# Kernel tuning notes

Hardware: AMD Instinct MI355X
Metric: run time of the kernel (lower is better)

The kernel has to match this reference:

```python
import jax, jax.numpy as jnp
import numpy as np

B, H, S, D = 4, 16, 1024, 64

def setup_inputs() -> dict:
    key = jax.random.key(0)
    kq, kk, kv, kb, km = jax.random.split(key, 5)
    return {
        "q": jax.random.normal(kq, (B, H, S, D), dtype=jnp.float32),
        "k": jax.random.normal(kk, (B, H, S, D), dtype=jnp.float32),
        "v": jax.random.normal(kv, (B, H, S, D), dtype=jnp.float32),
        "add_attn": jax.random.normal(kb, (B, 1, S, S), dtype=jnp.float32),
        "mask": jax.random.randint(km, (B, 1, 1, S), 0, 2, dtype=jnp.int32),
    }

def reference(q, k, v, add_attn, mask):
    d_emb = q.shape[-1]
    scale = 1.0 / jnp.sqrt(jnp.float32(d_emb)).astype(q.dtype)
    # scores: [B,H,Sq,Sk]
    attn = jnp.einsum('bhqd,bhkd->bhqk', q * scale, k)
    attn = attn + add_attn
    attn = jnp.where(mask == 0, jnp.asarray(-1e9, attn.dtype), attn)
    attn = jax.nn.softmax(attn, axis=-1)  # dropout with p=0 is identity
    output = jnp.einsum('bhqk,bhkd->bhqd', attn, v)
    return (output, attn)
```

## Files before the change

kernel.cpp:

```cpp
#include <hip/hip_runtime.h>
#include <math.h>

#define BB 4
#define HH 16
#define SS 1024
#define DD 64
#define QT 16
#define NKW 4
#define KPW 256

typedef __attribute__((ext_vector_type(8))) short bf16x8;
typedef __attribute__((ext_vector_type(4))) float f32x4;

static __device__ inline unsigned short f2bf(float f) {
    unsigned int u = __float_as_uint(f);
    u += 0x7fff + ((u >> 16) & 1);
    return (unsigned short)(u >> 16);
}

__global__ __launch_bounds__(256) void convert_qk(const float* __restrict__ q,
                                                  const float* __restrict__ k,
                                                  unsigned short* __restrict__ qb,
                                                  unsigned short* __restrict__ kb) {
    const int idx = blockIdx.x * 256 + threadIdx.x;
    float4 qv = ((const float4*)q)[idx];
    float4 kv = ((const float4*)k)[idx];
    ushort4 qo = make_ushort4(f2bf(qv.x), f2bf(qv.y), f2bf(qv.z), f2bf(qv.w));
    ushort4 ko = make_ushort4(f2bf(kv.x), f2bf(kv.y), f2bf(kv.z), f2bf(kv.w));
    ((ushort4*)qb)[idx] = qo;
    ((ushort4*)kb)[idx] = ko;
}

__global__ __launch_bounds__(256) void transpose_v(const float* __restrict__ v,
                                                   unsigned short* __restrict__ vt) {
    const int idx = blockIdx.x * 256 + threadIdx.x;
    const int k  = (idx & 255) * 4;
    const int d  = (idx >> 8) & 63;
    const int bh = idx >> 14;
    const float* vb = v + (size_t)bh * SS * DD;
    ushort4 o = make_ushort4(f2bf(vb[(size_t)(k + 0) * DD + d]),
                             f2bf(vb[(size_t)(k + 1) * DD + d]),
                             f2bf(vb[(size_t)(k + 2) * DD + d]),
                             f2bf(vb[(size_t)(k + 3) * DD + d]));
    ((ushort4*)vt)[idx] = o;
}

__global__ __launch_bounds__(256) void attn_mfma(
    const unsigned short* __restrict__ qb,
    const unsigned short* __restrict__ kb,
    const unsigned short* __restrict__ vtb,
    const float* __restrict__ add_attn,
    const int*   __restrict__ mask,
    float* __restrict__ out,
    float* __restrict__ attn_out)
{
    const int qt = blockIdx.x, h = blockIdx.y, b = blockIdx.z;
    const int bh = b * HH + h;
    const int tid = threadIdx.x;
    const int wave = tid >> 6;
    const int lane = tid & 63;
    const int col  = lane & 15;
    const int quad = lane >> 4;

    __shared__ unsigned short p_tile[NKW][QT][KPW + 8];
    __shared__ float red_m[NKW][QT];
    __shared__ float red_l[NKW][QT];
    __shared__ float o_part[NKW][QT][DD];

    const int q0  = qt * QT;
    const int wk0 = wave * KPW;

    const unsigned short* qrow = qb + ((size_t)bh * SS + q0 + col) * DD + quad * 8;
    const bf16x8 aq0 = *(const bf16x8*)(qrow);
    const bf16x8 aq1 = *(const bf16x8*)(qrow + 32);

    const unsigned short* kbb = kb + (size_t)bh * SS * DD;
    const float* bias = add_attn + ((size_t)b * SS + q0) * SS;
    const int*   mrow = mask + b * SS;

    float s[16][4];
#pragma unroll
    for (int t = 0; t < 16; ++t) {
        const int k0 = wk0 + t * 16;
        const unsigned short* kr = kbb + (size_t)(k0 + col) * DD + quad * 8;
        bf16x8 bk0 = *(const bf16x8*)(kr);
        bf16x8 bk1 = *(const bf16x8*)(kr + 32);
        f32x4 acc = {0.f, 0.f, 0.f, 0.f};
        acc = __builtin_amdgcn_mfma_f32_16x16x32_bf16(aq0, bk0, acc, 0, 0, 0);
        acc = __builtin_amdgcn_mfma_f32_16x16x32_bf16(aq1, bk1, acc, 0, 0, 0);
        const int kidx = k0 + col;
        const int mv = mrow[kidx];
#pragma unroll
        for (int r = 0; r < 4; ++r) {
            const int qr = quad * 4 + r;
            float sv = acc[r] * 0.125f + bias[(size_t)qr * SS + kidx];
            s[t][r] = (mv == 0) ? -1e9f : sv;
        }
    }

    float mx[4];
#pragma unroll
    for (int r = 0; r < 4; ++r) {
        float m = s[0][r];
#pragma unroll
        for (int t = 1; t < 16; ++t) m = fmaxf(m, s[t][r]);
        m = fmaxf(m, __shfl_xor(m, 1));
        m = fmaxf(m, __shfl_xor(m, 2));
        m = fmaxf(m, __shfl_xor(m, 4));
        m = fmaxf(m, __shfl_xor(m, 8));
        mx[r] = m;
    }
    if (col == 0) {
#pragma unroll
        for (int r = 0; r < 4; ++r) red_m[wave][quad * 4 + r] = mx[r];
    }
    __syncthreads();
    float mf[4];
#pragma unroll
    for (int r = 0; r < 4; ++r) {
        const int qr = quad * 4 + r;
        mf[r] = fmaxf(fmaxf(red_m[0][qr], red_m[1][qr]),
                      fmaxf(red_m[2][qr], red_m[3][qr]));
    }

    float ls[4] = {0.f, 0.f, 0.f, 0.f};
#pragma unroll
    for (int t = 0; t < 16; ++t) {
#pragma unroll
        for (int r = 0; r < 4; ++r) {
            float e = __expf(s[t][r] - mf[r]);
            s[t][r] = e;
            ls[r] += e;
        }
    }
#pragma unroll
    for (int r = 0; r < 4; ++r) {
        float l = ls[r];
        l += __shfl_xor(l, 1);
        l += __shfl_xor(l, 2);
        l += __shfl_xor(l, 4);
        l += __shfl_xor(l, 8);
        ls[r] = l;
    }
    if (col == 0) {
#pragma unroll
        for (int r = 0; r < 4; ++r) red_l[wave][quad * 4 + r] = ls[r];
    }
    __syncthreads();
    float inv[4];
#pragma unroll
    for (int r = 0; r < 4; ++r) {
        const int qr = quad * 4 + r;
        inv[r] = 1.0f / (red_l[0][qr] + red_l[1][qr] + red_l[2][qr] + red_l[3][qr]);
    }

    float* arow = attn_out + ((size_t)bh * SS + q0) * SS;
#pragma unroll
    for (int t = 0; t < 16; ++t) {
#pragma unroll
        for (int r = 0; r < 4; ++r) {
            const int qr = quad * 4 + r;
            float p = s[t][r] * inv[r];
            arow[(size_t)qr * SS + wk0 + t * 16 + col] = p;
            p_tile[wave][qr][t * 16 + col] = f2bf(p);
        }
    }

    const unsigned short* vt = vtb + (size_t)bh * DD * SS;
    f32x4 oacc[4];
#pragma unroll
    for (int dc = 0; dc < 4; ++dc) oacc[dc] = (f32x4){0.f, 0.f, 0.f, 0.f};
#pragma unroll
    for (int c = 0; c < 8; ++c) {
        bf16x8 ap = *(const bf16x8*)(&p_tile[wave][col][c * 32 + quad * 8]);
#pragma unroll
        for (int dc = 0; dc < 4; ++dc) {
            const unsigned short* vr =
                vt + (size_t)(dc * 16 + col) * SS + wk0 + c * 32 + quad * 8;
            bf16x8 bv = *(const bf16x8*)(vr);
            oacc[dc] = __builtin_amdgcn_mfma_f32_16x16x32_bf16(ap, bv, oacc[dc], 0, 0, 0);
        }
    }
#pragma unroll
    for (int dc = 0; dc < 4; ++dc)
#pragma unroll
        for (int r = 0; r < 4; ++r)
            o_part[wave][quad * 4 + r][dc * 16 + col] = oacc[dc][r];
    __syncthreads();

    for (int i = tid; i < QT * DD; i += 256) {
        const int qr = i >> 6, d = i & 63;
        out[((size_t)bh * SS + q0 + qr) * DD + d] =
            o_part[0][qr][d] + o_part[1][qr][d] + o_part[2][qr][d] + o_part[3][qr][d];
    }
}

extern "C" void kernel_launch(void* const* d_in, const int* in_sizes, int n_in,
                              void* d_out, int out_size, void* d_ws, size_t ws_size,
                              hipStream_t stream) {
    const float* q        = (const float*)d_in[0];
    const float* k        = (const float*)d_in[1];
    const float* v        = (const float*)d_in[2];
    const float* add_attn = (const float*)d_in[3];
    const int*   mask     = (const int*)d_in[4];

    float* out      = (float*)d_out;
    float* attn_out = (float*)d_out + (size_t)BB * HH * SS * DD;

    const size_t nelem = (size_t)BB * HH * SS * DD;
    unsigned short* qb  = (unsigned short*)d_ws;
    unsigned short* kbb = qb + nelem;
    unsigned short* vtb = kbb + nelem;

    convert_qk<<<dim3(nelem / 4 / 256), dim3(256), 0, stream>>>(q, k, qb, kbb);
    transpose_v<<<dim3(nelem / 4 / 256), dim3(256), 0, stream>>>(v, vtb);

    dim3 grid(SS / QT, HH, BB);
    attn_mfma<<<grid, dim3(256), 0, stream>>>(qb, kbb, vtb, add_attn, mask, out, attn_out);
}
```

Baseline: 474.4 us.

## Reuse bias/mask across heads per block, tile V transpose via LDS, nontemporal stores

Each attention block now handles 8 heads of one batch. The add_attn bias and mask tile is loaded into registers once and reused across those heads instead of being re-read per head. The V transpose goes through a shared-memory tile, so global reads and writes are coalesced. Outputs use nontemporal stores, and launch bounds request 2 blocks per CU. The grid shrinks to 64x2x4 blocks, which reduces parallelism, and the extra br[16][4] registers raise register pressure.

```diff
diff --git a/kernel.cpp b/kernel.cpp
--- a/kernel.cpp
+++ b/kernel.cpp
@@ -8,6 +8,7 @@
 #define QT 16
 #define NKW 4
 #define KPW 256
+#define HPB 8
 
 typedef __attribute__((ext_vector_type(8))) short bf16x8;
 typedef __attribute__((ext_vector_type(4))) float f32x4;
@@ -33,19 +34,36 @@
 
 __global__ __launch_bounds__(256) void transpose_v(const float* __restrict__ v,
                                                    unsigned short* __restrict__ vt) {
-    const int idx = blockIdx.x * 256 + threadIdx.x;
-    const int k  = (idx & 255) * 4;
-    const int d  = (idx >> 8) & 63;
-    const int bh = idx >> 14;
-    const float* vb = v + (size_t)bh * SS * DD;
-    ushort4 o = make_ushort4(f2bf(vb[(size_t)(k + 0) * DD + d]),
-                             f2bf(vb[(size_t)(k + 1) * DD + d]),
-                             f2bf(vb[(size_t)(k + 2) * DD + d]),
-                             f2bf(vb[(size_t)(k + 3) * DD + d]));
-    ((ushort4*)vt)[idx] = o;
-}
-
-__global__ __launch_bounds__(256) void attn_mfma(
+    __shared__ unsigned short t[DD][258];
+    const int bh = blockIdx.y;
+    const int k0 = blockIdx.x * 256;
+    const float* vb = v + ((size_t)bh * SS + k0) * DD;
+#pragma unroll
+    for (int j = 0; j < 16; ++j) {
+        const int f   = j * 256 + threadIdx.x;
+        const int row = f >> 4;
+        const int d4  = (f & 15) << 2;
+        float4 x = ((const float4*)vb)[f];
+        t[d4 + 0][row] = f2bf(x.x);
+        t[d4 + 1][row] = f2bf(x.y);
+        t[d4 + 2][row] = f2bf(x.z);
+        t[d4 + 3][row] = f2bf(x.w);
+    }
+    __syncthreads();
+    unsigned short* vo = vt + (size_t)bh * DD * SS + k0;
+#pragma unroll
+    for (int j = 0; j < 8; ++j) {
+        const int f  = j * 256 + threadIdx.x;
+        const int d  = f >> 5;
+        const int k8 = (f & 31) << 3;
+        const unsigned int* lp = (const unsigned int*)&t[d][k8];
+        uint4 w;
+        w.x = lp[0]; w.y = lp[1]; w.z = lp[2]; w.w = lp[3];
+        *(uint4*)(vo + (size_t)d * SS + k8) = w;
+    }
+}
+
+__global__ __launch_bounds__(256, 2) void attn_mfma(
     const unsigned short* __restrict__ qb,
     const unsigned short* __restrict__ kb,
     const unsigned short* __restrict__ vtb,
@@ -54,8 +72,7 @@
     float* __restrict__ out,
     float* __restrict__ attn_out)
 {
-    const int qt = blockIdx.x, h = blockIdx.y, b = blockIdx.z;
-    const int bh = b * HH + h;
+    const int qt = blockIdx.x, hg = blockIdx.y, b = blockIdx.z;
     const int tid = threadIdx.x;
     const int wave = tid >> 6;
     const int lane = tid & 63;
@@ -70,128 +87,143 @@
     const int q0  = qt * QT;
     const int wk0 = wave * KPW;
 
-    const unsigned short* qrow = qb + ((size_t)bh * SS + q0 + col) * DD + quad * 8;
-    const bf16x8 aq0 = *(const bf16x8*)(qrow);
-    const bf16x8 aq1 = *(const bf16x8*)(qrow + 32);
-
-    const unsigned short* kbb = kb + (size_t)bh * SS * DD;
     const float* bias = add_attn + ((size_t)b * SS + q0) * SS;
     const int*   mrow = mask + b * SS;
-
-    float s[16][4];
+    float br[16][4];
 #pragma unroll
     for (int t = 0; t < 16; ++t) {
-        const int k0 = wk0 + t * 16;
-        const unsigned short* kr = kbb + (size_t)(k0 + col) * DD + quad * 8;
-        bf16x8 bk0 = *(const bf16x8*)(kr);
-        bf16x8 bk1 = *(const bf16x8*)(kr + 32);
-        f32x4 acc = {0.f, 0.f, 0.f, 0.f};
-        acc = __builtin_amdgcn_mfma_f32_16x16x32_bf16(aq0, bk0, acc, 0, 0, 0);
-        acc = __builtin_amdgcn_mfma_f32_16x16x32_bf16(aq1, bk1, acc, 0, 0, 0);
-        const int kidx = k0 + col;
+        const int kidx = wk0 + t * 16 + col;
         const int mv = mrow[kidx];
 #pragma unroll
         for (int r = 0; r < 4; ++r) {
             const int qr = quad * 4 + r;
-            float sv = acc[r] * 0.125f + bias[(size_t)qr * SS + kidx];
-            s[t][r] = (mv == 0) ? -1e9f : sv;
-        }
-    }
-
-    float mx[4];
-#pragma unroll
-    for (int r = 0; r < 4; ++r) {
-        float m = s[0][r];
-#pragma unroll
-        for (int t = 1; t < 16; ++t) m = fmaxf(m, s[t][r]);
-        m = fmaxf(m, __shfl_xor(m, 1));
-        m = fmaxf(m, __shfl_xor(m, 2));
-        m = fmaxf(m, __shfl_xor(m, 4));
-        m = fmaxf(m, __shfl_xor(m, 8));
-        mx[r] = m;
-    }
-    if (col == 0) {
-#pragma unroll
-        for (int r = 0; r < 4; ++r) red_m[wave][quad * 4 + r] = mx[r];
-    }
-    __syncthreads();
-    float mf[4];
-#pragma unroll
-    for (int r = 0; r < 4; ++r) {
-        const int qr = quad * 4 + r;
-        mf[r] = fmaxf(fmaxf(red_m[0][qr], red_m[1][qr]),
-                      fmaxf(red_m[2][qr], red_m[3][qr]));
-    }
-
-    float ls[4] = {0.f, 0.f, 0.f, 0.f};
-#pragma unroll
-    for (int t = 0; t < 16; ++t) {
-#pragma unroll
-        for (int r = 0; r < 4; ++r) {
-            float e = __expf(s[t][r] - mf[r]);
-            s[t][r] = e;
-            ls[r] += e;
-        }
-    }
-#pragma unroll
-    for (int r = 0; r < 4; ++r) {
-        float l = ls[r];
-        l += __shfl_xor(l, 1);
-        l += __shfl_xor(l, 2);
-        l += __shfl_xor(l, 4);
-        l += __shfl_xor(l, 8);
-        ls[r] = l;
-    }
-    if (col == 0) {
-#pragma unroll
-        for (int r = 0; r < 4; ++r) red_l[wave][quad * 4 + r] = ls[r];
-    }
-    __syncthreads();
-    float inv[4];
-#pragma unroll
-    for (int r = 0; r < 4; ++r) {
-        const int qr = quad * 4 + r;
-        inv[r] = 1.0f / (red_l[0][qr] + red_l[1][qr] + red_l[2][qr] + red_l[3][qr]);
-    }
-
-    float* arow = attn_out + ((size_t)bh * SS + q0) * SS;
-#pragma unroll
-    for (int t = 0; t < 16; ++t) {
+            float bv = bias[(size_t)qr * SS + kidx];
+            br[t][r] = mv ? bv : -1e9f;
+        }
+    }
+
+    for (int hi = 0; hi < HPB; ++hi) {
+        const int h  = hg * HPB + hi;
+        const int bh = b * HH + h;
+
+        const unsigned short* qrow = qb + ((size_t)bh * SS + q0 + col) * DD + quad * 8;
+        const bf16x8 aq0 = *(const bf16x8*)(qrow);
+        const bf16x8 aq1 = *(const bf16x8*)(qrow + 32);
+
+        const unsigned short* kbb = kb + (size_t)bh * SS * DD;
+
+        float s[16][4];
+#pragma unroll
+        for (int t = 0; t < 16; ++t) {
+            const int k0 = wk0 + t * 16;
+            const unsigned short* kr = kbb + (size_t)(k0 + col) * DD + quad * 8;
+            bf16x8 bk0 = *(const bf16x8*)(kr);
+            bf16x8 bk1 = *(const bf16x8*)(kr + 32);
+            f32x4 acc = {0.f, 0.f, 0.f, 0.f};
+            acc = __builtin_amdgcn_mfma_f32_16x16x32_bf16(aq0, bk0, acc, 0, 0, 0);
+            acc = __builtin_amdgcn_mfma_f32_16x16x32_bf16(aq1, bk1, acc, 0, 0, 0);
+#pragma unroll
+            for (int r = 0; r < 4; ++r)
+                s[t][r] = acc[r] * 0.125f + br[t][r];
+        }
+
+        float mx[4];
+#pragma unroll
+        for (int r = 0; r < 4; ++r) {
+            float m = s[0][r];
+#pragma unroll
+            for (int t = 1; t < 16; ++t) m = fmaxf(m, s[t][r]);
+            m = fmaxf(m, __shfl_xor(m, 1));
+            m = fmaxf(m, __shfl_xor(m, 2));
+            m = fmaxf(m, __shfl_xor(m, 4));
+            m = fmaxf(m, __shfl_xor(m, 8));
+            mx[r] = m;
+        }
+        if (col == 0) {
+#pragma unroll
+            for (int r = 0; r < 4; ++r) red_m[wave][quad * 4 + r] = mx[r];
+        }
+        __syncthreads();
+        float mf[4];
 #pragma unroll
         for (int r = 0; r < 4; ++r) {
             const int qr = quad * 4 + r;
-            float p = s[t][r] * inv[r];
-            arow[(size_t)qr * SS + wk0 + t * 16 + col] = p;
-            p_tile[wave][qr][t * 16 + col] = f2bf(p);
-        }
-    }
-
-    const unsigned short* vt = vtb + (size_t)bh * DD * SS;
-    f32x4 oacc[4];
-#pragma unroll
-    for (int dc = 0; dc < 4; ++dc) oacc[dc] = (f32x4){0.f, 0.f, 0.f, 0.f};
-#pragma unroll
-    for (int c = 0; c < 8; ++c) {
-        bf16x8 ap = *(const bf16x8*)(&p_tile[wave][col][c * 32 + quad * 8]);
-#pragma unroll
-        for (int dc = 0; dc < 4; ++dc) {
-            const unsigned short* vr =
-                vt + (size_t)(dc * 16 + col) * SS + wk0 + c * 32 + quad * 8;
-            bf16x8 bv = *(const bf16x8*)(vr);
-            oacc[dc] = __builtin_amdgcn_mfma_f32_16x16x32_bf16(ap, bv, oacc[dc], 0, 0, 0);
-        }
-    }
-#pragma unroll
-    for (int dc = 0; dc < 4; ++dc)
-#pragma unroll
-        for (int r = 0; r < 4; ++r)
-            o_part[wave][quad * 4 + r][dc * 16 + col] = oacc[dc][r];
-    __syncthreads();
-
-    for (int i = tid; i < QT * DD; i += 256) {
-        const int qr = i >> 6, d = i & 63;
-        out[((size_t)bh * SS + q0 + qr) * DD + d] =
-            o_part[0][qr][d] + o_part[1][qr][d] + o_part[2][qr][d] + o_part[3][qr][d];
+            mf[r] = fmaxf(fmaxf(red_m[0][qr], red_m[1][qr]),
+                          fmaxf(red_m[2][qr], red_m[3][qr]));
+        }
+
+        float ls[4] = {0.f, 0.f, 0.f, 0.f};
+#pragma unroll
+        for (int t = 0; t < 16; ++t) {
+#pragma unroll
+            for (int r = 0; r < 4; ++r) {
+                float e = __expf(s[t][r] - mf[r]);
+                s[t][r] = e;
+                ls[r] += e;
+            }
+        }
+#pragma unroll
+        for (int r = 0; r < 4; ++r) {
+            float l = ls[r];
+            l += __shfl_xor(l, 1);
+            l += __shfl_xor(l, 2);
+            l += __shfl_xor(l, 4);
+            l += __shfl_xor(l, 8);
+            ls[r] = l;
+        }
+        if (col == 0) {
+#pragma unroll
+            for (int r = 0; r < 4; ++r) red_l[wave][quad * 4 + r] = ls[r];
+        }
+        __syncthreads();
+        float inv[4];
+#pragma unroll
+        for (int r = 0; r < 4; ++r) {
+            const int qr = quad * 4 + r;
+            inv[r] = 1.0f / (red_l[0][qr] + red_l[1][qr] + red_l[2][qr] + red_l[3][qr]);
+        }
+
+        float* arow = attn_out + ((size_t)bh * SS + q0) * SS;
+#pragma unroll
+        for (int t = 0; t < 16; ++t) {
+#pragma unroll
+            for (int r = 0; r < 4; ++r) {
+                const int qr = quad * 4 + r;
+                float p = s[t][r] * inv[r];
+                __builtin_nontemporal_store(p, &arow[(size_t)qr * SS + wk0 + t * 16 + col]);
+                p_tile[wave][qr][t * 16 + col] = f2bf(p);
+            }
+        }
+
+        const unsigned short* vt = vtb + (size_t)bh * DD * SS;
+        f32x4 oacc[4];
+#pragma unroll
+        for (int dc = 0; dc < 4; ++dc) oacc[dc] = (f32x4){0.f, 0.f, 0.f, 0.f};
+#pragma unroll
+        for (int c = 0; c < 8; ++c) {
+            bf16x8 ap = *(const bf16x8*)(&p_tile[wave][col][c * 32 + quad * 8]);
+#pragma unroll
+            for (int dc = 0; dc < 4; ++dc) {
+                const unsigned short* vr =
+                    vt + (size_t)(dc * 16 + col) * SS + wk0 + c * 32 + quad * 8;
+                bf16x8 bv = *(const bf16x8*)(vr);
+                oacc[dc] = __builtin_amdgcn_mfma_f32_16x16x32_bf16(ap, bv, oacc[dc], 0, 0, 0);
+            }
+        }
+#pragma unroll
+        for (int dc = 0; dc < 4; ++dc)
+#pragma unroll
+            for (int r = 0; r < 4; ++r)
+                o_part[wave][quad * 4 + r][dc * 16 + col] = oacc[dc][r];
+        __syncthreads();
+
+        for (int i = tid; i < QT * DD; i += 256) {
+            const int qr = i >> 6, d = i & 63;
+            float ov = o_part[0][qr][d] + o_part[1][qr][d] +
+                       o_part[2][qr][d] + o_part[3][qr][d];
+            __builtin_nontemporal_store(ov, &out[((size_t)bh * SS + q0 + qr) * DD + d]);
+        }
+        __syncthreads();
     }
 }
 
@@ -213,8 +245,8 @@
     unsigned short* vtb = kbb + nelem;
 
     convert_qk<<<dim3(nelem / 4 / 256), dim3(256), 0, stream>>>(q, k, qb, kbb);
-    transpose_v<<<dim3(nelem / 4 / 256), dim3(256), 0, stream>>>(v, vtb);
-
-    dim3 grid(SS / QT, HH, BB);
+    transpose_v<<<dim3(SS / 256, BB * HH), dim3(256), 0, stream>>>(v, vtb);
+
+    dim3 grid(SS / QT, 2, BB);
     attn_mfma<<<grid, dim3(256), 0, stream>>>(qb, kbb, vtb, add_attn, mask, out, attn_out);
 }
```

Measured after the change: 445.5 us. 1.06x faster.
